# Kernel optimization log

Hardware: AMD Instinct MI355X
Metric: run time of the kernel (lower is better)

The kernel has to match this reference:

```python
import jax, jax.numpy as jnp
import numpy as np

# Faithful JAX port of the approxmatch EMD kernel (Fan et al.) wrapped by emdDist.
# 10 soft-assignment (auction-style) iterations with annealed temperature level=-4^j,
# j = 7..-1, final iteration level = 0. match is accumulated transport mass;
# cost[b] = sum_{k,l} match[b,k,l] * ||x1_k - x2_l||.

_EPS = 1e-9


def _approxmatch(xyz1, xyz2):
    # xyz1: (b, n, 3), xyz2: (b, m, 3)
    b, n, _ = xyz1.shape
    m = xyz2.shape[1]
    factorl = max(n, m) / n
    factorr = max(n, m) / m
    remainL = jnp.full((b, n), factorl, dtype=xyz1.dtype)   # mass left on xyz1 points
    remainR = jnp.full((b, m), factorr, dtype=xyz1.dtype)   # capacity left on xyz2 points
    # pairwise squared distances (b, n, m)
    d2 = jnp.sum((xyz1[:, :, None, :] - xyz2[:, None, :, :]) ** 2, axis=-1)
    match = jnp.zeros((b, n, m), dtype=xyz1.dtype)
    for j in range(7, -3, -1):  # j = 7, 6, ..., -1, -2
        level = 0.0 if j == -2 else -(4.0 ** j)
        # proposal weights from each left point, scaled by remaining right capacity
        w = jnp.exp(level * d2) * remainR[:, None, :]                      # (b,n,m)
        w = w / (jnp.sum(w, axis=-1, keepdims=True) + _EPS) * remainL[:, :, None]
        # right points accept at most their remaining capacity
        sumr = jnp.sum(w, axis=1) + _EPS                                   # (b,m)
        ratio = jnp.minimum(remainR / sumr, 1.0)                           # (b,m)
        delta = w * ratio[:, None, :]                                      # accepted transfer
        match = match + delta
        remainL = jnp.maximum(remainL - jnp.sum(delta, axis=-1), 0.0)
        remainR = jnp.maximum(remainR - jnp.sum(delta, axis=1), 0.0)
    return match, d2


def setup_inputs() -> dict:
    key = jax.random.key(0)
    k1, k2 = jax.random.split(key)
    B, N, M = 8, 4096, 4096
    input1 = jax.random.normal(k1, (B, N, 3), dtype=jnp.float32)
    input2 = jax.random.normal(k2, (B, M, 3), dtype=jnp.float32)
    return {"input1": input1, "input2": input2}


def reference(input1, input2):
    match, d2 = _approxmatch(input1, input2)
    # original CUDA backward treats match as a constant -> stop_gradient
    match = jax.lax.stop_gradient(match)
    dist = jnp.sqrt(jnp.maximum(d2, 1e-12))
    cost = jnp.sum(match * dist, axis=(1, 2))  # (b,)
    return cost
```

## Files before the change

### kernel.cpp

```cpp
#include <hip/hip_runtime.h>

#define NPTS 4096
#define NB 8
#define TPB 256
#define MBLK 4
#define MAXCHUNK 1024
#define EPSC 1e-9f

#define EXP2(x)  __builtin_amdgcn_exp2f(x)
#define RCPF(x)  __builtin_amdgcn_rcpf(x)
#define SQRTF(x) __builtin_amdgcn_sqrtf(x)

template<int MODE, bool SKIP>
__global__ __launch_bounds__(TPB) void ca_kernel(
    const float* __restrict__ x1, const float* __restrict__ x2,
    float* __restrict__ dbuf,
    float* __restrict__ rsumP,
    const float* __restrict__ s0P,
    const float* __restrict__ s1P,
    float* __restrict__ rrbuf,
    float* __restrict__ costbuf,
    int iter, float c2cur, float c2next, int nseg, int chunk)
{
  __shared__ float4 x2s[MAXCHUNK];
  __shared__ float  rrs[MAXCHUNK];
  __shared__ float  red[TPB];

  const int tid    = threadIdx.x;
  const int nchunk = blockIdx.x;
  const int mseg   = blockIdx.y;
  const int b      = blockIdx.z;
  const int m0     = mseg * chunk;
  const int plane  = NB * NPTS;

  float cpart = 0.f;
  for (int mm = tid; mm < chunk; mm += TPB) {
    int m = m0 + mm;
    const float* q = x2 + ((size_t)b * NPTS + m) * 3;
    float qx = q[0], qy = q[1], qz = q[2];
    float u = 0.f, rrn = 1.f;
    if (MODE >= 1) {
      float s0 = 0.f;
      for (int s = 0; s < nseg; ++s) s0 += s0P[(s * NB + b) * NPTS + m];
      float rr    = (iter == 0) ? 1.f : rrbuf[(iter & 1) * plane + b * NPTS + m];
      float sumr  = fmaf(rr, s0, EPSC);
      float ratio = fminf(rr * RCPF(sumr), 1.f);
      u   = rr * ratio;
      rrn = fmaxf(rr - u * s0, 0.f);
      if (nchunk == 0) {
        rrbuf[((iter + 1) & 1) * plane + b * NPTS + m] = rrn;
        float s1 = 0.f;
        for (int s = 0; s < nseg; ++s) s1 += s1P[(s * NB + b) * NPTS + m];
        cpart += u * s1;
      }
    } else {
      if (nchunk == 0 && mseg == 0 && mm == 0) costbuf[b] = 0.f;
    }
    x2s[mm] = make_float4(qx, qy, qz, u);
    rrs[mm] = rrn;
  }
  if (MODE >= 1 && nchunk == 0) {
    red[tid] = cpart;
    __syncthreads();
    for (int s = TPB / 2; s > 0; s >>= 1) {
      if (tid < s) red[tid] += red[tid + s];
      __syncthreads();
    }
    if (tid == 0) atomicAdd(costbuf + b, red[0]);
  }
  __syncthreads();

  const int n0 = nchunk * (TPB * MBLK) + tid;
  float px[MBLK], py[MBLK], pz[MBLK], dacc[MBLK], racc[MBLK];
#pragma unroll
  for (int k = 0; k < MBLK; ++k) {
    const float* p = x1 + ((size_t)b * NPTS + n0 + k * TPB) * 3;
    px[k] = p[0]; py[k] = p[1]; pz[k] = p[2];
    dacc[k] = 0.f; racc[k] = 0.f;
  }

#pragma unroll 2
  for (int mm = 0; mm < chunk; ++mm) {
    float4 q  = x2s[mm];
    float rrv = rrs[mm];
    float argn[MBLK];
#pragma unroll
    for (int k = 0; k < MBLK; ++k) {
      float dx = px[k] - q.x, dy = py[k] - q.y, dz = pz[k] - q.z;
      float d2 = fmaf(dz, dz, fmaf(dy, dy, dx * dx));
      argn[k] = d2 * (MODE == 2 ? c2cur : c2next);
    }
    if (MODE <= 1) {
      bool go = true;
      if (SKIP) {
        float amax = argn[0];
#pragma unroll
        for (int k = 1; k < MBLK; ++k) amax = fmaxf(amax, argn[k]);
        go = amax > -126.f;
      }
      if (go) {
#pragma unroll
        for (int k = 0; k < MBLK; ++k) {
          float en = EXP2(argn[k]);
          dacc[k] = fmaf(en, rrv, dacc[k]);
          if (MODE == 1) { float e2 = en * en; racc[k] = fmaf(e2 * e2, q.w, racc[k]); }
        }
      }
    } else {
#pragma unroll
      for (int k = 0; k < MBLK; ++k) {
        dacc[k] += rrv;
        float ec = EXP2(argn[k]);
        racc[k] = fmaf(ec, q.w, racc[k]);
      }
    }
  }

  size_t dbase = ((size_t)(((iter + 1) & 1) * nseg + mseg) * NB + b) * NPTS;
  size_t rbase = ((size_t)mseg * NB + b) * NPTS;
#pragma unroll
  for (int k = 0; k < MBLK; ++k) {
    dbuf[dbase + n0 + k * TPB] = dacc[k];
    if (MODE >= 1) rsumP[rbase + n0 + k * TPB] = racc[k];
  }
}

template<bool SKIP>
__global__ __launch_bounds__(TPB) void b_kernel(
    const float* __restrict__ x1, const float* __restrict__ x2,
    const float* __restrict__ dbuf,
    const float* __restrict__ rsumP,
    float* __restrict__ s0P, float* __restrict__ s1P,
    float* __restrict__ lbuf,
    int iter, float c2, int nseg, int chunk)
{
  __shared__ float4 x1s[MAXCHUNK];

  const int tid    = threadIdx.x;
  const int mchunk = blockIdx.x;
  const int nsegi  = blockIdx.y;
  const int b      = blockIdx.z;
  const int nb0    = nsegi * chunk;
  const int plane  = NB * NPTS;

  for (int nn = tid; nn < chunk; nn += TPB) {
    int n = nb0 + nn;
    float dsum = 0.f;
    for (int s = 0; s < nseg; ++s)
      dsum += dbuf[(((iter & 1) * nseg + s) * NB + b) * NPTS + n];
    float rl;
    if (iter == 0) {
      rl = 1.f;
    } else {
      float rlp = lbuf[((iter - 1) & 1) * plane + b * NPTS + n];
      float dprev = 0.f;
      for (int s = 0; s < nseg; ++s)
        dprev += dbuf[((((iter - 1) & 1) * nseg + s) * NB + b) * NPTS + n];
      float ap = rlp * RCPF(dprev + EPSC);
      float rs = 0.f;
      for (int s = 0; s < nseg; ++s) rs += rsumP[(s * NB + b) * NPTS + n];
      rl = fmaxf(rlp - ap * rs, 0.f);
    }
    if (mchunk == 0) lbuf[(iter & 1) * plane + b * NPTS + n] = rl;
    float a = rl * RCPF(dsum + EPSC);
    const float* p = x1 + ((size_t)b * NPTS + n) * 3;
    x1s[nn] = make_float4(p[0], p[1], p[2], a);
  }
  __syncthreads();

  const int m0 = mchunk * (TPB * MBLK) + tid;
  float qx[MBLK], qy[MBLK], qz[MBLK], s0a[MBLK], s1a[MBLK];
#pragma unroll
  for (int k = 0; k < MBLK; ++k) {
    const float* q = x2 + ((size_t)b * NPTS + m0 + k * TPB) * 3;
    qx[k] = q[0]; qy[k] = q[1]; qz[k] = q[2];
    s0a[k] = 0.f; s1a[k] = 0.f;
  }

#pragma unroll 2
  for (int nn = 0; nn < chunk; ++nn) {
    float4 p = x1s[nn];
    float d2v[MBLK], arg[MBLK];
#pragma unroll
    for (int k = 0; k < MBLK; ++k) {
      float dx = p.x - qx[k], dy = p.y - qy[k], dz = p.z - qz[k];
      d2v[k] = fmaf(dz, dz, fmaf(dy, dy, dx * dx));
      arg[k] = d2v[k] * c2;
    }
    bool go = true;
    if (SKIP) {
      float amax = arg[0];
#pragma unroll
      for (int k = 1; k < MBLK; ++k) amax = fmaxf(amax, arg[k]);
      go = amax > -126.f;
    }
    if (go) {
#pragma unroll
      for (int k = 0; k < MBLK; ++k) {
        float e  = EXP2(arg[k]);
        float tt = p.w * e;
        s0a[k] += tt;
        s1a[k] = fmaf(tt, SQRTF(d2v[k]), s1a[k]);
      }
    }
  }

  size_t sbase = ((size_t)nsegi * NB + b) * NPTS;
#pragma unroll
  for (int k = 0; k < MBLK; ++k) {
    s0P[sbase + m0 + k * TPB] = s0a[k];
    s1P[sbase + m0 + k * TPB] = s1a[k];
  }
}

__global__ __launch_bounds__(TPB) void f_kernel(
    const float* __restrict__ s0P, const float* __restrict__ s1P,
    const float* __restrict__ rrbuf, float* __restrict__ costbuf, int nseg)
{
  __shared__ float red[TPB];
  const int b   = blockIdx.y;
  const int tid = threadIdx.x;
  const int m   = blockIdx.x * TPB + tid;
  const int plane = NB * NPTS;
  float s0 = 0.f, s1 = 0.f;
  for (int s = 0; s < nseg; ++s) {
    s0 += s0P[(s * NB + b) * NPTS + m];
    s1 += s1P[(s * NB + b) * NPTS + m];
  }
  float rr    = rrbuf[1 * plane + b * NPTS + m];
  float sumr  = fmaf(rr, s0, EPSC);
  float ratio = fminf(rr * RCPF(sumr), 1.f);
  red[tid] = rr * ratio * s1;
  __syncthreads();
  for (int s = TPB / 2; s > 0; s >>= 1) {
    if (tid < s) red[tid] += red[tid + s];
    __syncthreads();
  }
  if (tid == 0) atomicAdd(costbuf + b, red[0]);
}

__global__ void out_kernel(const float* __restrict__ costbuf,
                           float* __restrict__ out)
{
  int t = threadIdx.x;
  if (t < NB) out[t] = costbuf[t];
}

extern "C" void kernel_launch(void* const* d_in, const int* in_sizes, int n_in,
                              void* d_out, int out_size, void* d_ws, size_t ws_size,
                              hipStream_t stream) {
  const float* x1 = (const float*)d_in[0];
  const float* x2 = (const float*)d_in[1];
  float* out = (float*)d_out;

  const size_t plane = (size_t)NB * NPTS;
  int nseg = 32;
  while (nseg > 4 &&
         ((size_t)(5 * nseg + 4) * plane + NB) * sizeof(float) > ws_size)
    nseg >>= 1;
  const int chunk = NPTS / nseg;

  float* ws      = (float*)d_ws;
  float* dbuf    = ws;
  float* rsumP   = dbuf  + 2 * nseg * plane;
  float* s0P     = rsumP + nseg * plane;
  float* s1P     = s0P   + nseg * plane;
  float* lbuf    = s1P   + nseg * plane;
  float* rrbuf   = lbuf  + 2 * plane;
  float* costbuf = rrbuf + 2 * plane;

  const double L2E = 1.4426950408889634074;
  const double lv[10] = {-16384.0, -4096.0, -1024.0, -256.0, -64.0,
                         -16.0, -4.0, -1.0, -0.25, 0.0};
  float c2[10];
  for (int i = 0; i < 10; ++i) c2[i] = (float)(lv[i] * L2E);

  dim3 grid(NPTS / (TPB * MBLK), nseg, NB), blk(TPB);

  ca_kernel<0, true><<<grid, blk, 0, stream>>>(
      x1, x2, dbuf, rsumP, s0P, s1P, rrbuf, costbuf, -1, 0.f, c2[0], nseg, chunk);
  for (int i = 0; i < 10; ++i) {
    if (i <= 2)
      b_kernel<true><<<grid, blk, 0, stream>>>(
          x1, x2, dbuf, rsumP, s0P, s1P, lbuf, i, c2[i], nseg, chunk);
    else
      b_kernel<false><<<grid, blk, 0, stream>>>(
          x1, x2, dbuf, rsumP, s0P, s1P, lbuf, i, c2[i], nseg, chunk);
    if (i < 8) {
      if (i <= 1)
        ca_kernel<1, true><<<grid, blk, 0, stream>>>(
            x1, x2, dbuf, rsumP, s0P, s1P, rrbuf, costbuf, i, c2[i], c2[i + 1], nseg, chunk);
      else
        ca_kernel<1, false><<<grid, blk, 0, stream>>>(
            x1, x2, dbuf, rsumP, s0P, s1P, rrbuf, costbuf, i, c2[i], c2[i + 1], nseg, chunk);
    } else if (i == 8) {
      ca_kernel<2, false><<<grid, blk, 0, stream>>>(
          x1, x2, dbuf, rsumP, s0P, s1P, rrbuf, costbuf, 8, c2[8], 0.f, nseg, chunk);
    }
  }
  f_kernel<<<dim3(NPTS / TPB, NB), blk, 0, stream>>>(s0P, s1P, rrbuf, costbuf, nseg);
  out_kernel<<<dim3(1), dim3(64), 0, stream>>>(costbuf, out);
}
```

Before: 1.222 ms.

## Split partial-sum reductions into small kernels and prescale coordinates by temperature

Per-point reductions over segment partials (dsum, remaining mass, ratio, cost) move out of the heavy pairwise kernels into dedicated lightweight r1/r2 kernels. Each reduction is now done once per point rather than redundantly by every block. Coordinates are prescaled by sqrt(-level*log2e), so the inner loop computes exp2(-d2) without a multiply, and the sqrt term is rescaled at the end. The chunk size becomes a compile-time template parameter with deeper unrolling, up to 64 segments, and the final level-0 iteration gets a specialised path without exp. This adds more kernel launches and costs some precision in the scaled distances.

```diff
diff --git a/kernel.cpp b/kernel.cpp
--- a/kernel.cpp
+++ b/kernel.cpp
@@ -1,72 +1,42 @@
 #include <hip/hip_runtime.h>
 
 #define NPTS 4096
-#define NB 8
-#define TPB 256
+#define NB   8
+#define TPB  256
+#define TPBR 128
 #define MBLK 4
-#define MAXCHUNK 1024
 #define EPSC 1e-9f
 
 #define EXP2(x)  __builtin_amdgcn_exp2f(x)
 #define RCPF(x)  __builtin_amdgcn_rcpf(x)
 #define SQRTF(x) __builtin_amdgcn_sqrtf(x)
 
-template<int MODE, bool SKIP>
+template<int MODE, bool SKIP, int CHUNK>
 __global__ __launch_bounds__(TPB) void ca_kernel(
-    const float* __restrict__ x1, const float* __restrict__ x2,
-    float* __restrict__ dbuf,
+    const float* __restrict__ x2,
+    float* __restrict__ dbufP,
     float* __restrict__ rsumP,
-    const float* __restrict__ s0P,
-    const float* __restrict__ s1P,
-    float* __restrict__ rrbuf,
-    float* __restrict__ costbuf,
-    int iter, float c2cur, float c2next, int nseg, int chunk)
-{
-  __shared__ float4 x2s[MAXCHUNK];
-  __shared__ float  rrs[MAXCHUNK];
-  __shared__ float  red[TPB];
-
-  const int tid    = threadIdx.x;
-  const int nchunk = blockIdx.x;
-  const int mseg   = blockIdx.y;
-  const int b      = blockIdx.z;
-  const int m0     = mseg * chunk;
-  const int plane  = NB * NPTS;
-
-  float cpart = 0.f;
-  for (int mm = tid; mm < chunk; mm += TPB) {
+    const float* __restrict__ x1,
+    const float* __restrict__ ubuf,
+    const float* __restrict__ rrbuf,
+    float* __restrict__ out, float sc)
+{
+  __shared__ float4 x2s[CHUNK];
+  __shared__ float  rrs[CHUNK];
+
+  const int tid = threadIdx.x;
+  const int nchunk = blockIdx.x, mseg = blockIdx.y, b = blockIdx.z;
+  const int m0 = mseg * CHUNK;
+
+  if (MODE == 0 && nchunk == 0 && mseg == 0 && tid == 0) out[b] = 0.f;
+
+  for (int mm = tid; mm < CHUNK; mm += TPB) {
     int m = m0 + mm;
     const float* q = x2 + ((size_t)b * NPTS + m) * 3;
-    float qx = q[0], qy = q[1], qz = q[2];
     float u = 0.f, rrn = 1.f;
-    if (MODE >= 1) {
-      float s0 = 0.f;
-      for (int s = 0; s < nseg; ++s) s0 += s0P[(s * NB + b) * NPTS + m];
-      float rr    = (iter == 0) ? 1.f : rrbuf[(iter & 1) * plane + b * NPTS + m];
-      float sumr  = fmaf(rr, s0, EPSC);
-      float ratio = fminf(rr * RCPF(sumr), 1.f);
-      u   = rr * ratio;
-      rrn = fmaxf(rr - u * s0, 0.f);
-      if (nchunk == 0) {
-        rrbuf[((iter + 1) & 1) * plane + b * NPTS + m] = rrn;
-        float s1 = 0.f;
-        for (int s = 0; s < nseg; ++s) s1 += s1P[(s * NB + b) * NPTS + m];
-        cpart += u * s1;
-      }
-    } else {
-      if (nchunk == 0 && mseg == 0 && mm == 0) costbuf[b] = 0.f;
-    }
-    x2s[mm] = make_float4(qx, qy, qz, u);
+    if (MODE >= 1) { u = ubuf[b * NPTS + m]; rrn = rrbuf[b * NPTS + m]; }
+    x2s[mm] = make_float4(sc * q[0], sc * q[1], sc * q[2], u);
     rrs[mm] = rrn;
-  }
-  if (MODE >= 1 && nchunk == 0) {
-    red[tid] = cpart;
-    __syncthreads();
-    for (int s = TPB / 2; s > 0; s >>= 1) {
-      if (tid < s) red[tid] += red[tid + s];
-      __syncthreads();
-    }
-    if (tid == 0) atomicAdd(costbuf + b, red[0]);
   }
   __syncthreads();
 
@@ -75,96 +45,72 @@
 #pragma unroll
   for (int k = 0; k < MBLK; ++k) {
     const float* p = x1 + ((size_t)b * NPTS + n0 + k * TPB) * 3;
-    px[k] = p[0]; py[k] = p[1]; pz[k] = p[2];
+    px[k] = sc * p[0]; py[k] = sc * p[1]; pz[k] = sc * p[2];
     dacc[k] = 0.f; racc[k] = 0.f;
   }
 
-#pragma unroll 2
-  for (int mm = 0; mm < chunk; ++mm) {
+#pragma unroll 4
+  for (int mm = 0; mm < CHUNK; ++mm) {
     float4 q  = x2s[mm];
     float rrv = rrs[mm];
-    float argn[MBLK];
+    float ds2[MBLK];
 #pragma unroll
     for (int k = 0; k < MBLK; ++k) {
       float dx = px[k] - q.x, dy = py[k] - q.y, dz = pz[k] - q.z;
-      float d2 = fmaf(dz, dz, fmaf(dy, dy, dx * dx));
-      argn[k] = d2 * (MODE == 2 ? c2cur : c2next);
-    }
-    if (MODE <= 1) {
+      ds2[k] = fmaf(dz, dz, fmaf(dy, dy, dx * dx));
+    }
+    if (MODE == 2) {
+#pragma unroll
+      for (int k = 0; k < MBLK; ++k) {
+        dacc[k] += rrv;
+        float ec = EXP2(-ds2[k]);
+        racc[k] = fmaf(ec, q.w, racc[k]);
+      }
+    } else {
       bool go = true;
       if (SKIP) {
-        float amax = argn[0];
-#pragma unroll
-        for (int k = 1; k < MBLK; ++k) amax = fmaxf(amax, argn[k]);
-        go = amax > -126.f;
+        float dmin = ds2[0];
+#pragma unroll
+        for (int k = 1; k < MBLK; ++k) dmin = fminf(dmin, ds2[k]);
+        go = dmin < 126.f;
       }
       if (go) {
 #pragma unroll
         for (int k = 0; k < MBLK; ++k) {
-          float en = EXP2(argn[k]);
+          float en = EXP2(-ds2[k]);
           dacc[k] = fmaf(en, rrv, dacc[k]);
           if (MODE == 1) { float e2 = en * en; racc[k] = fmaf(e2 * e2, q.w, racc[k]); }
         }
       }
-    } else {
-#pragma unroll
-      for (int k = 0; k < MBLK; ++k) {
-        dacc[k] += rrv;
-        float ec = EXP2(argn[k]);
-        racc[k] = fmaf(ec, q.w, racc[k]);
-      }
-    }
-  }
-
-  size_t dbase = ((size_t)(((iter + 1) & 1) * nseg + mseg) * NB + b) * NPTS;
-  size_t rbase = ((size_t)mseg * NB + b) * NPTS;
+    }
+  }
+
+  size_t base = ((size_t)mseg * NB + b) * NPTS;
 #pragma unroll
   for (int k = 0; k < MBLK; ++k) {
-    dbuf[dbase + n0 + k * TPB] = dacc[k];
-    if (MODE >= 1) rsumP[rbase + n0 + k * TPB] = racc[k];
-  }
-}
-
-template<bool SKIP>
+    dbufP[base + n0 + k * TPB] = dacc[k];
+    if (MODE >= 1) rsumP[base + n0 + k * TPB] = racc[k];
+  }
+}
+
+template<int LVL0, bool SKIP, int CHUNK>
 __global__ __launch_bounds__(TPB) void b_kernel(
-    const float* __restrict__ x1, const float* __restrict__ x2,
-    const float* __restrict__ dbuf,
-    const float* __restrict__ rsumP,
+    const float* __restrict__ x1,
+    const float* __restrict__ abuf,
     float* __restrict__ s0P, float* __restrict__ s1P,
-    float* __restrict__ lbuf,
-    int iter, float c2, int nseg, int chunk)
-{
-  __shared__ float4 x1s[MAXCHUNK];
-
-  const int tid    = threadIdx.x;
-  const int mchunk = blockIdx.x;
-  const int nsegi  = blockIdx.y;
-  const int b      = blockIdx.z;
-  const int nb0    = nsegi * chunk;
-  const int plane  = NB * NPTS;
-
-  for (int nn = tid; nn < chunk; nn += TPB) {
-    int n = nb0 + nn;
-    float dsum = 0.f;
-    for (int s = 0; s < nseg; ++s)
-      dsum += dbuf[(((iter & 1) * nseg + s) * NB + b) * NPTS + n];
-    float rl;
-    if (iter == 0) {
-      rl = 1.f;
-    } else {
-      float rlp = lbuf[((iter - 1) & 1) * plane + b * NPTS + n];
-      float dprev = 0.f;
-      for (int s = 0; s < nseg; ++s)
-        dprev += dbuf[((((iter - 1) & 1) * nseg + s) * NB + b) * NPTS + n];
-      float ap = rlp * RCPF(dprev + EPSC);
-      float rs = 0.f;
-      for (int s = 0; s < nseg; ++s) rs += rsumP[(s * NB + b) * NPTS + n];
-      rl = fmaxf(rlp - ap * rs, 0.f);
-    }
-    if (mchunk == 0) lbuf[(iter & 1) * plane + b * NPTS + n] = rl;
-    float a = rl * RCPF(dsum + EPSC);
+    const float* __restrict__ x2, float sc, float inv_s)
+{
+  __shared__ float4 x1s[CHUNK];
+
+  const int tid = threadIdx.x;
+  const int mchunk = blockIdx.x, nsegi = blockIdx.y, b = blockIdx.z;
+  const int n0 = nsegi * CHUNK;
+
+  for (int nn = tid; nn < CHUNK; nn += TPB) {
+    int n = n0 + nn;
     const float* p = x1 + ((size_t)b * NPTS + n) * 3;
-    x1s[nn] = make_float4(p[0], p[1], p[2], a);
+    float a = abuf[b * NPTS + n];
+    x1s[nn] = make_float4(sc * p[0], sc * p[1], sc * p[2], a);
   }
   __syncthreads();
 
@@ -173,77 +119,181 @@
 #pragma unroll
   for (int k = 0; k < MBLK; ++k) {
     const float* q = x2 + ((size_t)b * NPTS + m0 + k * TPB) * 3;
-    qx[k] = q[0]; qy[k] = q[1]; qz[k] = q[2];
+    qx[k] = sc * q[0]; qy[k] = sc * q[1]; qz[k] = sc * q[2];
     s0a[k] = 0.f; s1a[k] = 0.f;
   }
 
-#pragma unroll 2
-  for (int nn = 0; nn < chunk; ++nn) {
+#pragma unroll 4
+  for (int nn = 0; nn < CHUNK; ++nn) {
     float4 p = x1s[nn];
-    float d2v[MBLK], arg[MBLK];
+    float ds2[MBLK];
 #pragma unroll
     for (int k = 0; k < MBLK; ++k) {
       float dx = p.x - qx[k], dy = p.y - qy[k], dz = p.z - qz[k];
-      d2v[k] = fmaf(dz, dz, fmaf(dy, dy, dx * dx));
-      arg[k] = d2v[k] * c2;
-    }
-    bool go = true;
-    if (SKIP) {
-      float amax = arg[0];
-#pragma unroll
-      for (int k = 1; k < MBLK; ++k) amax = fmaxf(amax, arg[k]);
-      go = amax > -126.f;
-    }
-    if (go) {
+      ds2[k] = fmaf(dz, dz, fmaf(dy, dy, dx * dx));
+    }
+    if (LVL0) {
 #pragma unroll
       for (int k = 0; k < MBLK; ++k) {
-        float e  = EXP2(arg[k]);
-        float tt = p.w * e;
-        s0a[k] += tt;
-        s1a[k] = fmaf(tt, SQRTF(d2v[k]), s1a[k]);
-      }
-    }
-  }
-
-  size_t sbase = ((size_t)nsegi * NB + b) * NPTS;
+        s0a[k] += p.w;
+        s1a[k] = fmaf(p.w, SQRTF(ds2[k]), s1a[k]);
+      }
+    } else {
+      bool go = true;
+      if (SKIP) {
+        float dmin = ds2[0];
+#pragma unroll
+        for (int k = 1; k < MBLK; ++k) dmin = fminf(dmin, ds2[k]);
+        go = dmin < 126.f;
+      }
+      if (go) {
+#pragma unroll
+        for (int k = 0; k < MBLK; ++k) {
+          float e  = EXP2(-ds2[k]);
+          float tt = p.w * e;
+          s0a[k] += tt;
+          s1a[k] = fmaf(tt, SQRTF(ds2[k]), s1a[k]);
+        }
+      }
+    }
+  }
+
+  size_t base = ((size_t)nsegi * NB + b) * NPTS;
 #pragma unroll
   for (int k = 0; k < MBLK; ++k) {
-    s0P[sbase + m0 + k * TPB] = s0a[k];
-    s1P[sbase + m0 + k * TPB] = s1a[k];
-  }
-}
-
-__global__ __launch_bounds__(TPB) void f_kernel(
+    s0P[base + m0 + k * TPB] = s0a[k];
+    s1P[base + m0 + k * TPB] = s1a[k] * inv_s;
+  }
+}
+
+template<int NSEG>
+__global__ __launch_bounds__(TPBR) void r1_kernel(
+    const float* __restrict__ dbufP, const float* __restrict__ rsumP,
+    float* __restrict__ lbuf, float* __restrict__ dtot,
+    float* __restrict__ abuf, int iter)
+{
+  const int idx = blockIdx.x * TPBR + threadIdx.x;
+  const int b = idx >> 12, n = idx & (NPTS - 1);
+  const int off = b * NPTS + n;
+
+  float dnew = 0.f;
+#pragma unroll
+  for (int s = 0; s < NSEG; ++s) dnew += dbufP[((size_t)s * NB + b) * NPTS + n];
+
+  float rl;
+  if (iter == 0) {
+    rl = 1.f;
+  } else {
+    float rlp = lbuf[off];
+    float ap  = rlp * RCPF(dtot[off] + EPSC);
+    float rs = 0.f;
+#pragma unroll
+    for (int s = 0; s < NSEG; ++s) rs += rsumP[((size_t)s * NB + b) * NPTS + n];
+    rl = fmaxf(rlp - ap * rs, 0.f);
+  }
+  lbuf[off] = rl;
+  dtot[off] = dnew;
+  abuf[off] = rl * RCPF(dnew + EPSC);
+}
+
+template<int NSEG, bool LAST>
+__global__ __launch_bounds__(TPBR) void r2_kernel(
     const float* __restrict__ s0P, const float* __restrict__ s1P,
-    const float* __restrict__ rrbuf, float* __restrict__ costbuf, int nseg)
-{
-  __shared__ float red[TPB];
-  const int b   = blockIdx.y;
-  const int tid = threadIdx.x;
-  const int m   = blockIdx.x * TPB + tid;
-  const int plane = NB * NPTS;
+    float* __restrict__ ubuf, float* __restrict__ rrbuf,
+    float* __restrict__ out, int iter)
+{
+  __shared__ float red[TPBR];
+  const int idx = blockIdx.x * TPBR + threadIdx.x;
+  const int b = idx >> 12, m = idx & (NPTS - 1);
+  const int off = b * NPTS + m;
+
   float s0 = 0.f, s1 = 0.f;
-  for (int s = 0; s < nseg; ++s) {
-    s0 += s0P[(s * NB + b) * NPTS + m];
-    s1 += s1P[(s * NB + b) * NPTS + m];
-  }
-  float rr    = rrbuf[1 * plane + b * NPTS + m];
+#pragma unroll
+  for (int s = 0; s < NSEG; ++s) {
+    s0 += s0P[((size_t)s * NB + b) * NPTS + m];
+    s1 += s1P[((size_t)s * NB + b) * NPTS + m];
+  }
+  float rr    = (iter == 0) ? 1.f : rrbuf[off];
   float sumr  = fmaf(rr, s0, EPSC);
   float ratio = fminf(rr * RCPF(sumr), 1.f);
-  red[tid] = rr * ratio * s1;
+  float u     = rr * ratio;
+  if (!LAST) {
+    ubuf[off]  = u;
+    rrbuf[off] = fmaxf(rr - u * s0, 0.f);
+  }
+
+  red[threadIdx.x] = u * s1;
   __syncthreads();
-  for (int s = TPB / 2; s > 0; s >>= 1) {
-    if (tid < s) red[tid] += red[tid + s];
+  for (int s = TPBR / 2; s > 0; s >>= 1) {
+    if (threadIdx.x < s) red[threadIdx.x] += red[threadIdx.x + s];
     __syncthreads();
   }
-  if (tid == 0) atomicAdd(costbuf + b, red[0]);
-}
-
-__global__ void out_kernel(const float* __restrict__ costbuf,
-                           float* __restrict__ out)
-{
-  int t = threadIdx.x;
-  if (t < NB) out[t] = costbuf[t];
+  if (threadIdx.x == 0) atomicAdd(out + b, red[0]);
+}
+
+template<int NSEG>
+static void run_all(const float* x1, const float* x2, float* out, float* ws,
+                    hipStream_t stream)
+{
+  constexpr int CHUNK = NPTS / NSEG;
+  const size_t plane = (size_t)NB * NPTS;
+
+  float* dbufP = ws;
+  float* rsumP = dbufP + (size_t)NSEG * plane;
+  float* s0P   = rsumP + (size_t)NSEG * plane;
+  float* s1P   = s0P   + (size_t)NSEG * plane;
+  float* dtot  = s1P   + (size_t)NSEG * plane;
+  float* lbuf  = dtot  + plane;
+  float* abuf  = lbuf  + plane;
+  float* ubuf  = abuf  + plane;
+  float* rrbuf = ubuf  + plane;
+
+  const double L2E = 1.4426950408889634074;
+  const double lv[10] = {-16384.0, -4096.0, -1024.0, -256.0, -64.0,
+                         -16.0, -4.0, -1.0, -0.25, 0.0};
+  float scl[10], inv_s[10];
+  for (int i = 0; i < 10; ++i) {
+    double c2 = lv[i] * L2E;
+    scl[i]   = (i == 9) ? 1.f : (float)sqrt(-c2);
+    inv_s[i] = (i == 9) ? 1.f : (float)(1.0 / sqrt(-c2));
+  }
+
+  dim3 gmain(NPTS / (TPB * MBLK), NSEG, NB), bmain(TPB);
+  dim3 gr(NPTS * NB / TPBR), br(TPBR);
+
+  ca_kernel<0, true, CHUNK><<<gmain, bmain, 0, stream>>>(
+      x2, dbufP, rsumP, x1, ubuf, rrbuf, out, scl[0]);
+
+  for (int i = 0; i < 10; ++i) {
+    r1_kernel<NSEG><<<gr, br, 0, stream>>>(dbufP, rsumP, lbuf, dtot, abuf, i);
+
+    if (i <= 2)
+      b_kernel<0, true, CHUNK><<<gmain, bmain, 0, stream>>>(
+          x1, abuf, s0P, s1P, x2, scl[i], inv_s[i]);
+    else if (i <= 8)
+      b_kernel<0, false, CHUNK><<<gmain, bmain, 0, stream>>>(
+          x1, abuf, s0P, s1P, x2, scl[i], inv_s[i]);
+    else
+      b_kernel<1, false, CHUNK><<<gmain, bmain, 0, stream>>>(
+          x1, abuf, s0P, s1P, x2, 1.f, 1.f);
+
+    if (i < 9)
+      r2_kernel<NSEG, false><<<gr, br, 0, stream>>>(s0P, s1P, ubuf, rrbuf, out, i);
+    else
+      r2_kernel<NSEG, true><<<gr, br, 0, stream>>>(s0P, s1P, ubuf, rrbuf, out, i);
+
+    if (i <= 7) {
+      if (i <= 1)
+        ca_kernel<1, true, CHUNK><<<gmain, bmain, 0, stream>>>(
+            x2, dbufP, rsumP, x1, ubuf, rrbuf, out, scl[i + 1]);
+      else
+        ca_kernel<1, false, CHUNK><<<gmain, bmain, 0, stream>>>(
+            x2, dbufP, rsumP, x1, ubuf, rrbuf, out, scl[i + 1]);
+    } else if (i == 8) {
+      ca_kernel<2, false, CHUNK><<<gmain, bmain, 0, stream>>>(
+          x2, dbufP, rsumP, x1, ubuf, rrbuf, out, scl[8]);
+    }
+  }
 }
 
 extern "C" void kernel_launch(void* const* d_in, const int* in_sizes, int n_in,
@@ -252,52 +302,14 @@
   const float* x1 = (const float*)d_in[0];
   const float* x2 = (const float*)d_in[1];
   float* out = (float*)d_out;
+  float* ws  = (float*)d_ws;
 
   const size_t plane = (size_t)NB * NPTS;
-  int nseg = 32;
-  while (nseg > 4 &&
-         ((size_t)(5 * nseg + 4) * plane + NB) * sizeof(float) > ws_size)
-    nseg >>= 1;
-  const int chunk = NPTS / nseg;
-
-  float* ws      = (float*)d_ws;
-  float* dbuf    = ws;
-  float* rsumP   = dbuf  + 2 * nseg * plane;
-  float* s0P     = rsumP + nseg * plane;
-  float* s1P     = s0P   + nseg * plane;
-  float* lbuf    = s1P   + nseg * plane;
-  float* rrbuf   = lbuf  + 2 * plane;
-  float* costbuf = rrbuf + 2 * plane;
-
-  const double L2E = 1.4426950408889634074;
-  const double lv[10] = {-16384.0, -4096.0, -1024.0, -256.0, -64.0,
-                         -16.0, -4.0, -1.0, -0.25, 0.0};
-  float c2[10];
-  for (int i = 0; i < 10; ++i) c2[i] = (float)(lv[i] * L2E);
-
-  dim3 grid(NPTS / (TPB * MBLK), nseg, NB), blk(TPB);
-
-  ca_kernel<0, true><<<grid, blk, 0, stream>>>(
-      x1, x2, dbuf, rsumP, s0P, s1P, rrbuf, costbuf, -1, 0.f, c2[0], nseg, chunk);
-  for (int i = 0; i < 10; ++i) {
-    if (i <= 2)
-      b_kernel<true><<<grid, blk, 0, stream>>>(
-          x1, x2, dbuf, rsumP, s0P, s1P, lbuf, i, c2[i], nseg, chunk);
-    else
-      b_kernel<false><<<grid, blk, 0, stream>>>(
-          x1, x2, dbuf, rsumP, s0P, s1P, lbuf, i, c2[i], nseg, chunk);
-    if (i < 8) {
-      if (i <= 1)
-        ca_kernel<1, true><<<grid, blk, 0, stream>>>(
-            x1, x2, dbuf, rsumP, s0P, s1P, rrbuf, costbuf, i, c2[i], c2[i + 1], nseg, chunk);
-      else
-        ca_kernel<1, false><<<grid, blk, 0, stream>>>(
-            x1, x2, dbuf, rsumP, s0P, s1P, rrbuf, costbuf, i, c2[i], c2[i + 1], nseg, chunk);
-    } else if (i == 8) {
-      ca_kernel<2, false><<<grid, blk, 0, stream>>>(
-          x1, x2, dbuf, rsumP, s0P, s1P, rrbuf, costbuf, 8, c2[8], 0.f, nseg, chunk);
-    }
-  }
-  f_kernel<<<dim3(NPTS / TPB, NB), blk, 0, stream>>>(s0P, s1P, rrbuf, costbuf, nseg);
-  out_kernel<<<dim3(1), dim3(64), 0, stream>>>(costbuf, out);
-}
+  auto need = [&](int nseg) {
+    return ((size_t)(4 * nseg + 5) * plane) * sizeof(float);
+  };
+
+  if (ws_size >= need(64))      run_all<64>(x1, x2, out, ws, stream);
+  else if (ws_size >= need(32)) run_all<32>(x1, x2, out, ws, stream);
+  else                          run_all<16>(x1, x2, out, ws, stream);
+}
```

Measured after the change: 1.034 ms. 1.18x faster.
